# Optimization experiments

Hardware: AMD Instinct MI355X
Metric: run time of the kernel (lower is better)

## Reference

```python
import jax, jax.numpy as jnp
import numpy as np
from jax import lax

H = 512
V = 32000
B = 64
S = 64
T = 32
TQ = 32
NUM_HOP = 3


def _p(key, shape, scale=0.05):
    return jax.random.normal(key, shape, dtype=jnp.float32) * scale


def setup_inputs() -> dict:
    key = jax.random.key(0)
    ks = jax.random.split(key, 20)
    inp = {}
    inp["contexts"] = jax.random.randint(ks[0], (B, S, T), 0, V)
    inp["questions"] = jax.random.randint(ks[1], (B, TQ), 0, V)
    inp["emb"] = _p(ks[2], (V, H), 1.0)
    # input module: bidirectional GRU (torch gate order r,z,n)
    inp["Wih_f"] = _p(ks[3], (3 * H, H)); inp["Whh_f"] = _p(ks[4], (3 * H, H))
    inp["bih_f"] = jnp.zeros((3 * H,), jnp.float32); inp["bhh_f"] = jnp.zeros((3 * H,), jnp.float32)
    inp["Wih_b"] = _p(ks[5], (3 * H, H)); inp["Whh_b"] = _p(ks[6], (3 * H, H))
    inp["bih_b"] = jnp.zeros((3 * H,), jnp.float32); inp["bhh_b"] = jnp.zeros((3 * H,), jnp.float32)
    # question module GRU
    inp["qWih"] = _p(ks[7], (3 * H, H)); inp["qWhh"] = _p(ks[8], (3 * H, H))
    inp["qbih"] = jnp.zeros((3 * H,), jnp.float32); inp["qbhh"] = jnp.zeros((3 * H,), jnp.float32)
    # attention GRU cell (note: source reuses br as both biases)
    inp["Wr"] = _p(ks[9], (H, H)); inp["Ur"] = _p(ks[10], (H, H)); inp["br"] = jnp.ones((H,), jnp.float32)
    inp["W"] = _p(ks[11], (H, H)); inp["U"] = _p(ks[12], (H, H))
    # episodic memory gate MLP + next-memory projection
    inp["z1_w"] = _p(ks[13], (H, 4 * H)); inp["z1_b"] = jnp.zeros((H,), jnp.float32)
    inp["z2_w"] = _p(ks[14], (1, H)); inp["z2_b"] = jnp.zeros((1,), jnp.float32)
    inp["nm_w"] = _p(ks[15], (H, 3 * H)); inp["nm_b"] = jnp.zeros((H,), jnp.float32)
    # answer module
    inp["ans_w"] = _p(ks[16], (V, 2 * H)); inp["ans_b"] = jnp.zeros((V,), jnp.float32)
    return inp


def _pos_enc(slen, elen):
    # l[s, e] = 1 - s/slen - (e/elen)*(1 - 2*s/slen); indexed by SENTENCE dim, as in source
    s = np.arange(slen, dtype=np.float64)[:, None]
    e = np.arange(elen, dtype=np.float64)[None, :]
    l = 1.0 - s / slen - (e / elen) * (1.0 - 2.0 * s / slen)
    return jnp.asarray(l, dtype=jnp.float32)  # (S, H)


def _gru(x, Wih, Whh, bih, bhh, reverse=False):
    # x: (B, T, H); torch nn.GRU math with gate order r, z, n
    Bn, Tn, Hn = x.shape
    h0 = jnp.zeros((Bn, Hn), x.dtype)

    def step(h, xt):
        gx = xt @ Wih.T + bih
        gh = h @ Whh.T + bhh
        xr, xz, xn = jnp.split(gx, 3, axis=-1)
        hr, hz, hn = jnp.split(gh, 3, axis=-1)
        r = jax.nn.sigmoid(xr + hr)
        z = jax.nn.sigmoid(xz + hz)
        n = jnp.tanh(xn + r * hn)
        h_new = (1.0 - z) * n + z * h
        return h_new, h_new

    h_last, hs = lax.scan(step, h0, jnp.swapaxes(x, 0, 1), reverse=reverse)
    return jnp.swapaxes(hs, 0, 1), h_last


def _dmn(emb, Wih_f, Whh_f, bih_f, bhh_f, Wih_b, Whh_b, bih_b, bhh_b,
         qWih, qWhh, qbih, qbhh, Wr, Ur, br, W, U,
         z1_w, z1_b, z2_w, z2_b, nm_w, nm_b, ans_w, ans_b,
         contexts, questions):
    emb0 = emb.at[0].set(0.0)  # padding_idx=0
    Bn, Sn, Tn = contexts.shape
    Hn = emb.shape[1]
    # ---- input module ----
    ce = emb0[contexts]                                   # (B,S,T,H)
    pe = _pos_enc(Sn, Hn)                                 # (S,H), broadcast over tokens (faithful)
    facts_in = jnp.sum(ce * pe[None, :, None, :], axis=2)  # (B,S,H)
    hf, _ = _gru(facts_in, Wih_f, Whh_f, bih_f, bhh_f, reverse=False)
    hb, _ = _gru(facts_in, Wih_b, Whh_b, bih_b, bhh_b, reverse=True)
    facts = hf + hb                                       # (B,S,H); dropout = identity (eval)
    # ---- question module ----
    _, q = _gru(emb0[questions], qWih, qWhh, qbih, qbhh)  # (B,H)
    # ---- episodic memory hops ----
    facts_t = jnp.swapaxes(facts, 0, 1)                   # (S,B,H)
    M = q
    for _ in range(NUM_HOP):
        qb = q[:, None, :]
        Mb = M[:, None, :]
        z = jnp.concatenate([facts * qb, facts * Mb,
                             jnp.abs(facts - qb), jnp.abs(facts - Mb)], axis=-1)  # (B,S,4H)
        g1 = jnp.tanh(z @ z1_w.T + z1_b)
        G = jax.nn.softmax((g1 @ z2_w.T + z2_b)[..., 0], axis=1)  # (B,S)

        def agru(c, sg):
            fact, g = sg
            r = jax.nn.sigmoid(fact @ Wr + c @ Ur + br)
            ht = jnp.tanh(fact @ W + r * (c @ U) + br)  # source reuses br as b
            return g[:, None] * ht + (1.0 - g[:, None]) * c, None

        C, _ = lax.scan(agru, jnp.zeros((Bn, Hn), facts.dtype), (facts_t, G.T))
        M = jax.nn.relu(jnp.concatenate([M, C, q], axis=-1) @ nm_w.T + nm_b)
    # ---- answer module (dropout = identity) ----
    preds = jnp.concatenate([M, q], axis=-1) @ ans_w.T + ans_b  # (B,V)
    return preds


def reference(contexts, questions, emb, Wih_f, Whh_f, bih_f, bhh_f,
              Wih_b, Whh_b, bih_b, bhh_b, qWih, qWhh, qbih, qbhh,
              Wr, Ur, br, W, U, z1_w, z1_b, z2_w, z2_b, nm_w, nm_b,
              ans_w, ans_b):
    return _dmn(emb, Wih_f, Whh_f, bih_f, bhh_f, Wih_b, Whh_b, bih_b, bhh_b,
                qWih, qWhh, qbih, qbhh, Wr, Ur, br, W, U,
                z1_w, z1_b, z2_w, z2_b, nm_w, nm_b, ans_w, ans_b,
                contexts, questions)
```

## Files before the change

kernel.cpp:

```cpp
#include <hip/hip_runtime.h>
#include <cstddef>
#include <cstdint>

namespace {

constexpr int H  = 512;
constexpr int V  = 32000;
constexpr int B  = 64;
constexpr int S  = 64;
constexpr int T  = 32;
constexpr int TQ = 32;

typedef unsigned short ushort_t;
typedef __attribute__((ext_vector_type(8))) short bf16x8;
typedef __attribute__((ext_vector_type(4))) short bf16x4;
typedef __attribute__((ext_vector_type(4))) float f32x4;

__device__ __forceinline__ ushort_t f2bf(float f) {
  union { float f; unsigned u; } v; v.f = f;
  return (ushort_t)((v.u + 0x7FFFu + ((v.u >> 16) & 1u)) >> 16);
}

__device__ __forceinline__ float sigm(float x) { return 1.f / (1.f + expf(-x)); }

__device__ __forceinline__ bf16x8 pack8(f32x4 a, f32x4 b) {
  bf16x8 r;
  r[0] = (short)f2bf(a[0]); r[1] = (short)f2bf(a[1]);
  r[2] = (short)f2bf(a[2]); r[3] = (short)f2bf(a[3]);
  r[4] = (short)f2bf(b[0]); r[5] = (short)f2bf(b[1]);
  r[6] = (short)f2bf(b[2]); r[7] = (short)f2bf(b[3]);
  return r;
}
__device__ __forceinline__ bf16x4 pack4(f32x4 a) {
  bf16x4 r;
  r[0] = (short)f2bf(a[0]); r[1] = (short)f2bf(a[1]);
  r[2] = (short)f2bf(a[2]); r[3] = (short)f2bf(a[3]);
  return r;
}

__device__ __forceinline__ f32x4 load4c(const float* p) {
  f32x4 v;
  asm volatile("global_load_dwordx4 %0, %1, off sc0 sc1" : "=v"(v) : "v"(p));
  return v;
}
__device__ __forceinline__ float load1c(const float* p) {
  float v;
  asm volatile("global_load_dword %0, %1, off sc0 sc1" : "=v"(v) : "v"(p));
  return v;
}
__device__ __forceinline__ void store1c(float* p, float v) {
  asm volatile("global_store_dword %0, %1, off sc0 sc1" :: "v"(p), "v"(v) : "memory");
}
__device__ __forceinline__ void store1cu(unsigned* p, unsigned v) {
  asm volatile("global_store_dword %0, %1, off sc0 sc1" :: "v"(p), "v"(v) : "memory");
}
__device__ __forceinline__ void waitvm0() {
  asm volatile("s_waitcnt vmcnt(0)" ::: "memory");
  __builtin_amdgcn_sched_barrier(0);
}

__device__ __forceinline__ void flag_barrier(unsigned* flags, int rank,
                                             unsigned step1, int t, int lane, int wv) {
  waitvm0();
  __syncthreads();
  if (t == 0) store1cu(flags + rank * 32, step1);
  if (wv == 0) {
    const unsigned* fp = flags + (lane & 7) * 32;
    for (;;) {
      unsigned v;
      asm volatile("global_load_dword %0, %1, off sc0 sc1" : "=v"(v) : "v"(fp));
      asm volatile("s_waitcnt vmcnt(0)" ::: "memory");
      const int ok = (lane >= 8) || (v >= step1);
      if (__all(ok)) break;
      __builtin_amdgcn_s_sleep(1);
    }
  }
  __syncthreads();
}

__global__ __launch_bounds__(256) void k_embed_facts(const int* __restrict__ ctx,
                                                     const float* __restrict__ emb,
                                                     float* __restrict__ facts_in) {
  const int bs = blockIdx.x;
  const int s  = bs & (S - 1);
  const int t  = threadIdx.x;
  __shared__ int sidx[T];
  if (t < T) sidx[t] = ctx[(size_t)bs * T + t];
  __syncthreads();
  float a0 = 0.f, a1 = 0.f;
  for (int tt = 0; tt < T; ++tt) {
    const int ix = sidx[tt];
    if (ix != 0) {
      const float* e = emb + ((size_t)ix << 9);
      a0 += e[t];
      a1 += e[t + 256];
    }
  }
  const float sf = (float)s * (1.f / 64.f);
  const float c1 = 1.f - sf;
  const float c2 = (1.f - 2.f * sf) * (1.f / 512.f);
  facts_in[((size_t)bs << 9) + t]       = a0 * (c1 - (float)t * c2);
  facts_in[((size_t)bs << 9) + t + 256] = a1 * (c1 - (float)(t + 256) * c2);
}

__global__ __launch_bounds__(256) void k_embed_q(const int* __restrict__ qidx,
                                                 const float* __restrict__ emb,
                                                 float* __restrict__ qe) {
  const int bt = blockIdx.x;
  const int t  = threadIdx.x;
  const int ix = qidx[bt];
  float v0 = 0.f, v1 = 0.f;
  if (ix != 0) {
    const float* e = emb + ((size_t)ix << 9);
    v0 = e[t];
    v1 = e[t + 256];
  }
  qe[((size_t)bt << 9) + t]       = v0;
  qe[((size_t)bt << 9) + t + 256] = v1;
}

__global__ __launch_bounds__(256) void k_transpose512(const float* __restrict__ src,
                                                      float* __restrict__ dst) {
  __shared__ float tile[32][33];
  const int x0 = blockIdx.x * 32, y0 = blockIdx.y * 32;
  for (int i = threadIdx.y; i < 32; i += 8)
    tile[i][threadIdx.x] = src[(size_t)(y0 + i) * H + x0 + threadIdx.x];
  __syncthreads();
  for (int i = threadIdx.y; i < 32; i += 8)
    dst[(size_t)(x0 + i) * H + y0 + threadIdx.x] = tile[threadIdx.x][i];
}

template <int ACT>
__global__ __launch_bounds__(256) void k_gemm_mfma(const float* __restrict__ Af,
                                                   const float* __restrict__ Bm,
                                                   const float* __restrict__ bias,
                                                   float* __restrict__ C,
                                                   int M, int N, int K) {
  __shared__ __align__(16) ushort_t As[64][72];
  __shared__ __align__(16) ushort_t Bs[64][72];
  const int t    = threadIdx.x;
  const int lane = t & 63;
  const int w    = t >> 6;
  const int wr   = w >> 1, wc = w & 1;
  const int m0 = blockIdx.y << 6, n0 = blockIdx.x << 6;
  const int row = t >> 2;
  const int ch  = t & 3;

  f32x4 acc[2][2] = {};

  for (int k0 = 0; k0 < K; k0 += 64) {
#pragma unroll
    for (int cc = 0; cc < 2; ++cc) {
      const int c8 = ch + cc * 4;
      const float* src = Af + (size_t)(m0 + row) * K + k0 + c8 * 8;
      *(bf16x8*)&As[row][c8 * 8] = pack8(*(const f32x4*)src, *(const f32x4*)(src + 4));
      const float* srb = Bm + (size_t)(n0 + row) * K + k0 + c8 * 8;
      *(bf16x8*)&Bs[row][c8 * 8] = pack8(*(const f32x4*)srb, *(const f32x4*)(srb + 4));
    }
    __syncthreads();
#pragma unroll
    for (int ks = 0; ks < 2; ++ks) {
      bf16x8 a[2], b[2];
#pragma unroll
      for (int fr = 0; fr < 2; ++fr)
        a[fr] = *(const bf16x8*)&As[wr * 32 + fr * 16 + (lane & 15)][ks * 32 + (lane >> 4) * 8];
#pragma unroll
      for (int fc = 0; fc < 2; ++fc)
        b[fc] = *(const bf16x8*)&Bs[wc * 32 + fc * 16 + (lane & 15)][ks * 32 + (lane >> 4) * 8];
#pragma unroll
      for (int fr = 0; fr < 2; ++fr)
#pragma unroll
        for (int fc = 0; fc < 2; ++fc)
          acc[fr][fc] = __builtin_amdgcn_mfma_f32_16x16x32_bf16(a[fr], b[fc], acc[fr][fc], 0, 0, 0);
    }
    __syncthreads();
  }
#pragma unroll
  for (int fr = 0; fr < 2; ++fr) {
#pragma unroll
    for (int fc = 0; fc < 2; ++fc) {
      const int rbase = m0 + wr * 32 + fr * 16 + ((lane >> 4) << 2);
      const int col   = n0 + wc * 32 + fc * 16 + (lane & 15);
      const float bv  = bias ? bias[col] : 0.f;
#pragma unroll
      for (int j = 0; j < 4; ++j) {
        float v = acc[fr][fc][j] + bv;
        if (ACT == 1) v = tanhf(v);
        if (ACT == 2) v = fmaxf(v, 0.f);
        C[(size_t)(rbase + j) * N + col] = v;
      }
    }
  }
}

__global__ __launch_bounds__(256) void k_gemm_z1(const float* __restrict__ facts,
                                                 const float* __restrict__ qv,
                                                 const float* __restrict__ Mv,
                                                 const float* __restrict__ Bm,
                                                 const float* __restrict__ bias,
                                                 float* __restrict__ C) {
  constexpr int N = 512, K = 2048;
  __shared__ __align__(16) ushort_t As[64][72];
  __shared__ __align__(16) ushort_t Bs[64][72];
  const int t    = threadIdx.x;
  const int lane = t & 63;
  const int w    = t >> 6;
  const int wr   = w >> 1, wc = w & 1;
  const int m0 = blockIdx.y << 6, n0 = blockIdx.x << 6;
  const int row = t >> 2;
  const int ch  = t & 3;
  const int b   = blockIdx.y;

  f32x4 acc[2][2] = {};

  for (int k0 = 0; k0 < K; k0 += 64) {
    const int seg = k0 >> 9;
    const int kb  = k0 & 511;
    const float* other = ((seg & 1) ? Mv : qv) + ((size_t)b << 9);
#pragma unroll
    for (int cc = 0; cc < 2; ++cc) {
      const int c8 = ch + cc * 4;
      const int kk = kb + c8 * 8;
      const float* fp = facts + ((size_t)(m0 + row) << 9) + kk;
      const f32x4 f0 = *(const f32x4*)fp;
      const f32x4 f1 = *(const f32x4*)(fp + 4);
      const f32x4 o0 = *(const f32x4*)(other + kk);
      const f32x4 o1 = *(const f32x4*)(other + kk + 4);
      f32x4 z0, z1;
      if (seg < 2) {
        z0 = f0 * o0; z1 = f1 * o1;
      } else {
        z0 = f0 - o0; z1 = f1 - o1;
#pragma unroll
        for (int e = 0; e < 4; ++e) { z0[e] = fabsf(z0[e]); z1[e] = fabsf(z1[e]); }
      }
      *(bf16x8*)&As[row][c8 * 8] = pack8(z0, z1);
      const float* srb = Bm + (size_t)(n0 + row) * K + k0 + c8 * 8;
      *(bf16x8*)&Bs[row][c8 * 8] = pack8(*(const f32x4*)srb, *(const f32x4*)(srb + 4));
    }
    __syncthreads();
#pragma unroll
    for (int ks = 0; ks < 2; ++ks) {
      bf16x8 a[2], bb[2];
#pragma unroll
      for (int fr = 0; fr < 2; ++fr)
        a[fr] = *(const bf16x8*)&As[wr * 32 + fr * 16 + (lane & 15)][ks * 32 + (lane >> 4) * 8];
#pragma unroll
      for (int fc = 0; fc < 2; ++fc)
        bb[fc] = *(const bf16x8*)&Bs[wc * 32 + fc * 16 + (lane & 15)][ks * 32 + (lane >> 4) * 8];
#pragma unroll
      for (int fr = 0; fr < 2; ++fr)
#pragma unroll
        for (int fc = 0; fc < 2; ++fc)
          acc[fr][fc] = __builtin_amdgcn_mfma_f32_16x16x32_bf16(a[fr], bb[fc], acc[fr][fc], 0, 0, 0);
    }
    __syncthreads();
  }
#pragma unroll
  for (int fr = 0; fr < 2; ++fr) {
#pragma unroll
    for (int fc = 0; fc < 2; ++fc) {
      const int rbase = m0 + wr * 32 + fr * 16 + ((lane >> 4) << 2);
      const int col   = n0 + wc * 32 + fc * 16 + (lane & 15);
      const float bv  = bias[col];
#pragma unroll
      for (int j = 0; j < 4; ++j)
        C[(size_t)(rbase + j) * N + col] = tanhf(acc[fr][fc][j] + bv);
    }
  }
}

__global__ __launch_bounds__(256) void k_gemm_cat3(const float* __restrict__ Mv,
                                                   const float* __restrict__ Cv,
                                                   const float* __restrict__ qv,
                                                   const float* __restrict__ Bm,
                                                   const float* __restrict__ bias,
                                                   float* __restrict__ C) {
  constexpr int N = 512, K = 1536;
  __shared__ __align__(16) ushort_t As[64][72];
  __shared__ __align__(16) ushort_t Bs[64][72];
  const int t    = threadIdx.x;
  const int lane = t & 63;
  const int w    = t >> 6;
  const int wr   = w >> 1, wc = w & 1;
  const int n0 = blockIdx.x << 6;
  const int row = t >> 2;
  const int ch  = t & 3;

  f32x4 acc[2][2] = {};

  for (int k0 = 0; k0 < K; k0 += 64) {
    const int seg = k0 >> 9;
    const float* src = (seg == 0) ? Mv : (seg == 1) ? Cv : qv;
    const int kb = k0 & 511;
#pragma unroll
    for (int cc = 0; cc < 2; ++cc) {
      const int c8 = ch + cc * 4;
      const float* fp = src + ((size_t)row << 9) + kb + c8 * 8;
      *(bf16x8*)&As[row][c8 * 8] = pack8(*(const f32x4*)fp, *(const f32x4*)(fp + 4));
      const float* srb = Bm + (size_t)(n0 + row) * K + k0 + c8 * 8;
      *(bf16x8*)&Bs[row][c8 * 8] = pack8(*(const f32x4*)srb, *(const f32x4*)(srb + 4));
    }
    __syncthreads();
#pragma unroll
    for (int ks = 0; ks < 2; ++ks) {
      bf16x8 a[2], bb[2];
#pragma unroll
      for (int fr = 0; fr < 2; ++fr)
        a[fr] = *(const bf16x8*)&As[wr * 32 + fr * 16 + (lane & 15)][ks * 32 + (lane >> 4) * 8];
#pragma unroll
      for (int fc = 0; fc < 2; ++fc)
        bb[fc] = *(const bf16x8*)&Bs[wc * 32 + fc * 16 + (lane & 15)][ks * 32 + (lane >> 4) * 8];
#pragma unroll
      for (int fr = 0; fr < 2; ++fr)
#pragma unroll
        for (int fc = 0; fc < 2; ++fc)
          acc[fr][fc] = __builtin_amdgcn_mfma_f32_16x16x32_bf16(a[fr], bb[fc], acc[fr][fc], 0, 0, 0);
    }
    __syncthreads();
  }
#pragma unroll
  for (int fr = 0; fr < 2; ++fr) {
#pragma unroll
    for (int fc = 0; fc < 2; ++fc) {
      const int rbase = wr * 32 + fr * 16 + ((lane >> 4) << 2);
      const int col   = n0 + wc * 32 + fc * 16 + (lane & 15);
      const float bv  = bias[col];
#pragma unroll
      for (int j = 0; j < 4; ++j)
        C[(size_t)(rbase + j) * N + col] = fmaxf(acc[fr][fc][j] + bv, 0.f);
    }
  }
}

__global__ __launch_bounds__(256) void k_gemm_cat2(const float* __restrict__ Mv,
                                                   const float* __restrict__ qv,
                                                   const float* __restrict__ Bm,
                                                   const float* __restrict__ bias,
                                                   float* __restrict__ C) {
  constexpr int N = 32000, K = 1024;
  __shared__ __align__(16) ushort_t As[64][72];
  __shared__ __align__(16) ushort_t Bs[64][72];
  const int t    = threadIdx.x;
  const int lane = t & 63;
  const int w    = t >> 6;
  const int wr   = w >> 1, wc = w & 1;
  const int n0 = blockIdx.x << 6;
  const int row = t >> 2;
  const int ch  = t & 3;

  f32x4 acc[2][2] = {};

  for (int k0 = 0; k0 < K; k0 += 64) {
    const float* src = (k0 < 512) ? Mv : qv;
    const int kb = k0 & 511;
#pragma unroll
    for (int cc = 0; cc < 2; ++cc) {
      const int c8 = ch + cc * 4;
      const float* fp = src + ((size_t)row << 9) + kb + c8 * 8;
      *(bf16x8*)&As[row][c8 * 8] = pack8(*(const f32x4*)fp, *(const f32x4*)(fp + 4));
      const float* srb = Bm + (size_t)(n0 + row) * K + k0 + c8 * 8;
      *(bf16x8*)&Bs[row][c8 * 8] = pack8(*(const f32x4*)srb, *(const f32x4*)(srb + 4));
    }
    __syncthreads();
#pragma unroll
    for (int ks = 0; ks < 2; ++ks) {
      bf16x8 a[2], bb[2];
#pragma unroll
      for (int fr = 0; fr < 2; ++fr)
        a[fr] = *(const bf16x8*)&As[wr * 32 + fr * 16 + (lane & 15)][ks * 32 + (lane >> 4) * 8];
#pragma unroll
      for (int fc = 0; fc < 2; ++fc)
        bb[fc] = *(const bf16x8*)&Bs[wc * 32 + fc * 16 + (lane & 15)][ks * 32 + (lane >> 4) * 8];
#pragma unroll
      for (int fr = 0; fr < 2; ++fr)
#pragma unroll
        for (int fc = 0; fc < 2; ++fc)
          acc[fr][fc] = __builtin_amdgcn_mfma_f32_16x16x32_bf16(a[fr], bb[fc], acc[fr][fc], 0, 0, 0);
    }
    __syncthreads();
  }
#pragma unroll
  for (int fr = 0; fr < 2; ++fr) {
#pragma unroll
    for (int fc = 0; fc < 2; ++fc) {
      const int rbase = wr * 32 + fr * 16 + ((lane >> 4) << 2);
      const int col   = n0 + wc * 32 + fc * 16 + (lane & 15);
      const float bv  = bias[col];
#pragma unroll
      for (int j = 0; j < 4; ++j)
        C[(size_t)(rbase + j) * N + col] = acc[fr][fc][j] + bv;
    }
  }
}

__global__ __launch_bounds__(256, 1) void k_gru_scan_mfma(
    const float* __restrict__ Whh_f, const float* __restrict__ bhh_f,
    const float* __restrict__ Whh_b, const float* __restrict__ bhh_b,
    const float* __restrict__ qWhh,  const float* __restrict__ qbhh,
    const float* __restrict__ gx_f, const float* __restrict__ gx_b,
    const float* __restrict__ gx_q,
    float* __restrict__ Hbuf, float* __restrict__ facts,
    float* __restrict__ hb_all, unsigned* __restrict__ flags_base) {
  const int bx   = blockIdx.x;
  const int grp  = bx >> 3;
  const int rank = bx & 7;
  const int gru  = grp >> 2;
  const int ib   = grp & 3;

  const float* Whh; const float* bhh; const float* gx;
  float* H0; float* H1; float* out_seq; int seqlen, rev;
  if (gru == 0)      { Whh = Whh_f; bhh = bhh_f; gx = gx_f; H0 = Hbuf;          H1 = Hbuf + 32768;  out_seq = facts;   seqlen = S;  rev = 0; }
  else if (gru == 1) { Whh = Whh_b; bhh = bhh_b; gx = gx_b; H0 = Hbuf + 65536;  H1 = Hbuf + 98304;  out_seq = hb_all;  seqlen = S;  rev = 1; }
  else               { Whh = qWhh;  bhh = qbhh;  gx = gx_q; H0 = Hbuf + 131072; H1 = Hbuf + 163840; out_seq = nullptr; seqlen = TQ; rev = 0; }

  __shared__ __align__(16) ushort_t hl[16 * 520];

  const int t    = threadIdx.x;
  const int lane = t & 63;
  const int wv   = t >> 6;
  const int nt   = (rank << 2) + wv;
  const int lm   = lane & 15;
  const int lk   = lane >> 4;
  const int col  = (nt << 4) + lm;

  bf16x8 wf[3][16];
#pragma unroll
  for (int g = 0; g < 3; ++g) {
    const float* wrow = Whh + ((size_t)(g * 512 + col) << 9) + (lk << 3);
#pragma unroll
    for (int ks = 0; ks < 16; ++ks) {
      const float* p = wrow + ks * 32;
      wf[g][ks] = pack8(*(const f32x4*)p, *(const f32x4*)(p + 4));
    }
  }
  const float bv0 = bhh[col], bv1 = bhh[512 + col], bv2 = bhh[1024 + col];
  unsigned* flags = flags_base + grp * 8 * 32;

  float xr[4], xz[4], xn[4];
  {
    const int xidx = rev ? (seqlen - 1) : 0;
#pragma unroll
    for (int j = 0; j < 4; ++j) {
      const int b = (ib << 4) + (lk << 2) + j;
      const size_t gxrow = ((size_t)b * seqlen + xidx) * 1536;
      xr[j] = gx[gxrow + col];
      xz[j] = gx[gxrow + 512 + col];
      xn[j] = gx[gxrow + 1024 + col];
    }
  }

  for (int s = 0; s < seqlen; ++s) {
    float hp[4] = {0.f, 0.f, 0.f, 0.f};
    if (s == 0) {
      for (int i = t; i < 4160; i += 256) ((unsigned*)hl)[i] = 0u;
    } else {
      const float* Hp = (s & 1) ? H1 : H0;
      f32x4 v[8];
#pragma unroll
      for (int u = 0; u < 8; ++u) {
        const int i = (u << 8) + t;
        v[u] = load4c(Hp + ((size_t)((ib << 4) + (i >> 7)) << 9) + ((i & 127) << 2));
      }
#pragma unroll
      for (int j = 0; j < 4; ++j)
        hp[j] = load1c(Hp + ((size_t)((ib << 4) + (lk << 2) + j) << 9) + col);
      waitvm0();
#pragma unroll
      for (int u = 0; u < 8; ++u) {
        const int i = (u << 8) + t;
        *(bf16x4*)&hl[(i >> 7) * 520 + ((i & 127) << 2)] = pack4(v[u]);
      }
    }
    __syncthreads();

    f32x4 acc0 = {}, acc1 = {}, acc2 = {};
#pragma unroll
    for (int ks = 0; ks < 16; ++ks) {
      const bf16x8 a = *(const bf16x8*)&hl[lm * 520 + (ks << 5) + (lk << 3)];
      acc0 = __builtin_amdgcn_mfma_f32_16x16x32_bf16(a, wf[0][ks], acc0, 0, 0, 0);
      acc1 = __builtin_amdgcn_mfma_f32_16x16x32_bf16(a, wf[1][ks], acc1, 0, 0, 0);
      acc2 = __builtin_amdgcn_mfma_f32_16x16x32_bf16(a, wf[2][ks], acc2, 0, 0, 0);
    }

    const int xidx = rev ? (seqlen - 1 - s) : s;
    float* Hn = (s & 1) ? H0 : H1;
#pragma unroll
    for (int j = 0; j < 4; ++j) {
      const int b = (ib << 4) + (lk << 2) + j;
      const float r = sigm(xr[j] + acc0[j] + bv0);
      const float z = sigm(xz[j] + acc1[j] + bv1);
      const float n = tanhf(xn[j] + r * (acc2[j] + bv2));
      const float hnew = (1.f - z) * n + z * hp[j];
      store1c(Hn + ((size_t)b << 9) + col, hnew);
      if (out_seq) out_seq[((size_t)(b * S + xidx) << 9) + col] = hnew;
    }

    if (s + 1 < seqlen) {
      const int xidx2 = rev ? (seqlen - 2 - s) : (s + 1);
      float nxr[4], nxz[4], nxn[4];
#pragma unroll
      for (int j = 0; j < 4; ++j) {
        const int b = (ib << 4) + (lk << 2) + j;
        const size_t gxrow = ((size_t)b * seqlen + xidx2) * 1536;
        nxr[j] = gx[gxrow + col];
        nxz[j] = gx[gxrow + 512 + col];
        nxn[j] = gx[gxrow + 1024 + col];
      }
      flag_barrier(flags, rank, (unsigned)(s + 1), t, lane, wv);
#pragma unroll
      for (int j = 0; j < 4; ++j) { xr[j] = nxr[j]; xz[j] = nxz[j]; xn[j] = nxn[j]; }
    }
  }
}

__global__ __launch_bounds__(256, 1) void k_agru_scan_mfma(
    const float* __restrict__ UrT, const float* __restrict__ UT,
    const float* __restrict__ fRW, const float* __restrict__ fW,
    const float* __restrict__ br, const float* __restrict__ G,
    float* __restrict__ C0, float* __restrict__ C1,
    unsigned* __restrict__ flags_base) {
  const int bx   = blockIdx.x;
  const int grp  = bx >> 3;
  const int rank = bx & 7;

  __shared__ __align__(16) ushort_t cl[16 * 520];

  const int t    = threadIdx.x;
  const int lane = t & 63;
  const int wv   = t >> 6;
  const int nt   = (rank << 2) + wv;
  const int lm   = lane & 15;
  const int lk   = lane >> 4;
  const int col  = (nt << 4) + lm;

  bf16x8 wfr[16], wfu[16];
  {
    const float* r0 = UrT + ((size_t)col << 9) + (lk << 3);
    const float* r1 = UT  + ((size_t)col << 9) + (lk << 3);
#pragma unroll
    for (int ks = 0; ks < 16; ++ks) {
      wfr[ks] = pack8(*(const f32x4*)(r0 + ks * 32), *(const f32x4*)(r0 + ks * 32 + 4));
      wfu[ks] = pack8(*(const f32x4*)(r1 + ks * 32), *(const f32x4*)(r1 + ks * 32 + 4));
    }
  }
  const float brv = br[col];
  unsigned* flags = flags_base + grp * 8 * 32;

  float fr[4], fw[4], gg[4];
#pragma unroll
  for (int j = 0; j < 4; ++j) {
    const int b = (grp << 4) + (lk << 2) + j;
    const size_t fi = ((size_t)(b * S) << 9) + col;
    fr[j] = fRW[fi];
    fw[j] = fW[fi];
    gg[j] = G[b << 6];
  }

  for (int s = 0; s < S; ++s) {
    float cp[4] = {0.f, 0.f, 0.f, 0.f};
    if (s == 0) {
      for (int i = t; i < 4160; i += 256) ((unsigned*)cl)[i] = 0u;
    } else {
      const float* Cp = (s & 1) ? C1 : C0;
      f32x4 v[8];
#pragma unroll
      for (int u = 0; u < 8; ++u) {
        const int i = (u << 8) + t;
        v[u] = load4c(Cp + ((size_t)((grp << 4) + (i >> 7)) << 9) + ((i & 127) << 2));
      }
#pragma unroll
      for (int j = 0; j < 4; ++j)
        cp[j] = load1c(Cp + ((size_t)((grp << 4) + (lk << 2) + j) << 9) + col);
      waitvm0();
#pragma unroll
      for (int u = 0; u < 8; ++u) {
        const int i = (u << 8) + t;
        *(bf16x4*)&cl[(i >> 7) * 520 + ((i & 127) << 2)] = pack4(v[u]);
      }
    }
    __syncthreads();

    f32x4 accr = {}, accu = {};
#pragma unroll
    for (int ks = 0; ks < 16; ++ks) {
      const bf16x8 a = *(const bf16x8*)&cl[lm * 520 + (ks << 5) + (lk << 3)];
      accr = __builtin_amdgcn_mfma_f32_16x16x32_bf16(a, wfr[ks], accr, 0, 0, 0);
      accu = __builtin_amdgcn_mfma_f32_16x16x32_bf16(a, wfu[ks], accu, 0, 0, 0);
    }

    float* Cn = (s & 1) ? C0 : C1;
#pragma unroll
    for (int j = 0; j < 4; ++j) {
      const int b = (grp << 4) + (lk << 2) + j;
      const float r  = sigm(fr[j] + accr[j] + brv);
      const float ht = tanhf(fw[j] + r * accu[j] + brv);
      store1c(Cn + ((size_t)b << 9) + col, gg[j] * ht + (1.f - gg[j]) * cp[j]);
    }

    if (s + 1 < S) {
      float nfr[4], nfw[4], ngg[4];
#pragma unroll
      for (int j = 0; j < 4; ++j) {
        const int b = (grp << 4) + (lk << 2) + j;
        const size_t fi = ((size_t)(b * S + s + 1) << 9) + col;
        nfr[j] = fRW[fi];
        nfw[j] = fW[fi];
        ngg[j] = G[(b << 6) + s + 1];
      }
      flag_barrier(flags, rank, (unsigned)(s + 1), t, lane, wv);
#pragma unroll
      for (int j = 0; j < 4; ++j) { fr[j] = nfr[j]; fw[j] = nfw[j]; gg[j] = ngg[j]; }
    }
  }
}

__global__ __launch_bounds__(256) void k_add(float* __restrict__ a, const float* __restrict__ b) {
  const size_t i = (((size_t)blockIdx.x << 8) + threadIdx.x) << 2;
  float4 x = *(float4*)(a + i);
  const float4 y = *(const float4*)(b + i);
  x.x += y.x; x.y += y.y; x.z += y.z; x.w += y.w;
  *(float4*)(a + i) = x;
}

__global__ __launch_bounds__(256) void k_score_softmax(const float* __restrict__ g1,
                                                       const float* __restrict__ z2w,
                                                       const float* __restrict__ z2b,
                                                       float* __restrict__ G) {
  const int b = blockIdx.x, t = threadIdx.x;
  const int wave = t >> 6, lane = t & 63;
  __shared__ float sc[64];
  for (int si = 0; si < 16; ++si) {
    const int s = wave * 16 + si;
    const float* row = g1 + ((size_t)(b * S + s) << 9) + lane * 8;
    const float* w   = z2w + lane * 8;
    float p = 0.f;
#pragma unroll
    for (int k = 0; k < 8; ++k) p += row[k] * w[k];
#pragma unroll
    for (int off = 32; off; off >>= 1) p += __shfl_xor(p, off);
    if (lane == 0) sc[s] = p + z2b[0];
  }
  __syncthreads();
  if (wave == 0) {
    const float v = sc[lane];
    float m = v;
#pragma unroll
    for (int off = 32; off; off >>= 1) m = fmaxf(m, __shfl_xor(m, off));
    const float e = expf(v - m);
    float su = e;
#pragma unroll
    for (int off = 32; off; off >>= 1) su += __shfl_xor(su, off);
    G[(b << 6) + lane] = e / su;
  }
}

}

extern "C" void kernel_launch(void* const* d_in, const int* in_sizes, int n_in,
                              void* d_out, int out_size, void* d_ws, size_t ws_size,
                              hipStream_t stream) {
  const int*   contexts  = (const int*)d_in[0];
  const int*   questions = (const int*)d_in[1];
  const float* emb   = (const float*)d_in[2];
  const float* Wih_f = (const float*)d_in[3];
  const float* Whh_f = (const float*)d_in[4];
  const float* bih_f = (const float*)d_in[5];
  const float* bhh_f = (const float*)d_in[6];
  const float* Wih_b = (const float*)d_in[7];
  const float* Whh_b = (const float*)d_in[8];
  const float* bih_b = (const float*)d_in[9];
  const float* bhh_b = (const float*)d_in[10];
  const float* qWih  = (const float*)d_in[11];
  const float* qWhh  = (const float*)d_in[12];
  const float* qbih  = (const float*)d_in[13];
  const float* qbhh  = (const float*)d_in[14];
  const float* Wr    = (const float*)d_in[15];
  const float* Ur    = (const float*)d_in[16];
  const float* br    = (const float*)d_in[17];
  const float* Wm    = (const float*)d_in[18];
  const float* Um    = (const float*)d_in[19];
  const float* z1_w  = (const float*)d_in[20];
  const float* z1_b  = (const float*)d_in[21];
  const float* z2_w  = (const float*)d_in[22];
  const float* z2_b  = (const float*)d_in[23];
  const float* nm_w  = (const float*)d_in[24];
  const float* nm_b  = (const float*)d_in[25];
  const float* ans_w = (const float*)d_in[26];
  const float* ans_b = (const float*)d_in[27];
  (void)in_sizes; (void)n_in; (void)out_size; (void)ws_size;

  float* ws = (float*)d_ws;
  float* WrT      = ws + 0;
  float* UrT      = ws + 262144;
  float* WT       = ws + 524288;
  float* UT       = ws + 786432;
  float* facts_in = ws + 1048576;
  float* qe       = ws + 3145728;
  float* gx_f     = ws + 4194304;
  float* gx_b     = ws + 10485760;
  float* gx_q     = ws + 16777216;
  float* facts    = ws + 19922944;
  float* hb       = ws + 22020096;
  float* Hbuf     = ws + 24117248;
  float* C0       = ws + 24313856;
  float* C1       = ws + 24346624;
  float* M0       = ws + 24379392;
  float* M1       = ws + 24412160;
  float* Mq       = ws + 24543232;
  float* Gm       = ws + 24608768;
  float* g1  = gx_q;
  float* fRW = facts_in;
  float* fW  = hb;
  float* preds = (float*)d_out;
  unsigned* bar = (unsigned*)Mq;

  float* q = Hbuf + 131072;

  hipMemsetAsync(bar, 0, 6144 * sizeof(unsigned), stream);

  k_embed_facts<<<B * S, 256, 0, stream>>>(contexts, emb, facts_in);
  k_embed_q<<<B * TQ, 256, 0, stream>>>(questions, emb, qe);
  dim3 tb(32, 8);
  k_transpose512<<<dim3(16, 16), tb, 0, stream>>>(Wr, WrT);
  k_transpose512<<<dim3(16, 16), tb, 0, stream>>>(Ur, UrT);
  k_transpose512<<<dim3(16, 16), tb, 0, stream>>>(Wm, WT);
  k_transpose512<<<dim3(16, 16), tb, 0, stream>>>(Um, UT);

  k_gemm_mfma<0><<<dim3(24, 64), 256, 0, stream>>>(facts_in, Wih_f, bih_f, gx_f, 4096, 1536, 512);
  k_gemm_mfma<0><<<dim3(24, 64), 256, 0, stream>>>(facts_in, Wih_b, bih_b, gx_b, 4096, 1536, 512);
  k_gemm_mfma<0><<<dim3(24, 32), 256, 0, stream>>>(qe, qWih, qbih, gx_q, 2048, 1536, 512);

  k_gru_scan_mfma<<<96, 256, 0, stream>>>(Whh_f, bhh_f, Whh_b, bhh_b, qWhh, qbhh,
                                          gx_f, gx_b, gx_q, Hbuf, facts, hb, bar);
  k_add<<<2048, 256, 0, stream>>>(facts, hb);

  k_gemm_mfma<0><<<dim3(8, 64), 256, 0, stream>>>(facts, WrT, nullptr, fRW, 4096, 512, 512);
  k_gemm_mfma<0><<<dim3(8, 64), 256, 0, stream>>>(facts, WT,  nullptr, fW,  4096, 512, 512);

  const float* Mcur = q;
  for (int h = 0; h < 3; ++h) {
    k_gemm_z1<<<dim3(8, 64), 256, 0, stream>>>(facts, q, Mcur, z1_w, z1_b, g1);
    k_score_softmax<<<B, 256, 0, stream>>>(g1, z2_w, z2_b, Gm);
    unsigned* fl = bar + 3072 + h * 1024;
    k_agru_scan_mfma<<<32, 256, 0, stream>>>(UrT, UT, fRW, fW, br, Gm, C0, C1, fl);
    float* Mnext = (h & 1) ? M1 : M0;
    k_gemm_cat3<<<dim3(8, 1), 256, 0, stream>>>(Mcur, C0, q, nm_w, nm_b, Mnext);
    Mcur = Mnext;
  }

  k_gemm_cat2<<<dim3(500, 1), 256, 0, stream>>>(Mcur, q, ans_w, ans_b, preds);
}
```

Before: 1.585 ms.

## Exchange recurrent hidden state as bf16 and keep own state in registers

The GRU and attention-GRU scans now publish each step's hidden state to global memory as bf16 instead of fp32. Each block keeps its own previous values in registers rather than reloading them, which halves the per-step cross-block traffic on the serial critical path. Separately, the z1 gate GEMM is split into a kernel that builds the concatenated features as bf16, followed by the generic MFMA GEMM with a bf16 A path. That split adds an extra kernel launch and a write/read of a 4096x2048 bf16 buffer on each hop.

New measurement: 1.400 ms. 1.13x faster.

```diff
diff --git a/kernel.cpp b/kernel.cpp
--- a/kernel.cpp
+++ b/kernel.cpp
@@ -15,6 +15,7 @@
 typedef __attribute__((ext_vector_type(8))) short bf16x8;
 typedef __attribute__((ext_vector_type(4))) short bf16x4;
 typedef __attribute__((ext_vector_type(4))) float f32x4;
+typedef __attribute__((ext_vector_type(4))) unsigned u32x4;
 
 __device__ __forceinline__ ushort_t f2bf(float f) {
   union { float f; unsigned u; } v; v.f = f;
@@ -31,25 +32,14 @@
   r[6] = (short)f2bf(b[2]); r[7] = (short)f2bf(b[3]);
   return r;
 }
-__device__ __forceinline__ bf16x4 pack4(f32x4 a) {
-  bf16x4 r;
-  r[0] = (short)f2bf(a[0]); r[1] = (short)f2bf(a[1]);
-  r[2] = (short)f2bf(a[2]); r[3] = (short)f2bf(a[3]);
-  return r;
-}
-
-__device__ __forceinline__ f32x4 load4c(const float* p) {
-  f32x4 v;
+
+__device__ __forceinline__ u32x4 load16c(const void* p) {
+  u32x4 v;
   asm volatile("global_load_dwordx4 %0, %1, off sc0 sc1" : "=v"(v) : "v"(p));
   return v;
 }
-__device__ __forceinline__ float load1c(const float* p) {
-  float v;
-  asm volatile("global_load_dword %0, %1, off sc0 sc1" : "=v"(v) : "v"(p));
-  return v;
-}
-__device__ __forceinline__ void store1c(float* p, float v) {
-  asm volatile("global_store_dword %0, %1, off sc0 sc1" :: "v"(p), "v"(v) : "memory");
+__device__ __forceinline__ void store2c(ushort_t* p, unsigned v) {
+  asm volatile("global_store_short %0, %1, off sc0 sc1" :: "v"(p), "v"(v) : "memory");
 }
 __device__ __forceinline__ void store1cu(unsigned* p, unsigned v) {
   asm volatile("global_store_dword %0, %1, off sc0 sc1" :: "v"(p), "v"(v) : "memory");
@@ -130,8 +120,8 @@
     dst[(size_t)(x0 + i) * H + y0 + threadIdx.x] = tile[threadIdx.x][i];
 }
 
-template <int ACT>
-__global__ __launch_bounds__(256) void k_gemm_mfma(const float* __restrict__ Af,
+template <bool A_BF16, int ACT>
+__global__ __launch_bounds__(256) void k_gemm_mfma(const void* __restrict__ Av,
                                                    const float* __restrict__ Bm,
                                                    const float* __restrict__ bias,
                                                    float* __restrict__ C,
@@ -149,11 +139,26 @@
   f32x4 acc[2][2] = {};
 
   for (int k0 = 0; k0 < K; k0 += 64) {
+    if (A_BF16) {
+      const ushort_t* A16 = (const ushort_t*)Av;
+#pragma unroll
+      for (int cc = 0; cc < 2; ++cc) {
+        const int c8 = ch + cc * 4;
+        const uint4 v = *(const uint4*)(A16 + (size_t)(m0 + row) * K + k0 + c8 * 8);
+        *(uint4*)&As[row][c8 * 8] = v;
+      }
+    } else {
+      const float* Af = (const float*)Av;
+#pragma unroll
+      for (int cc = 0; cc < 2; ++cc) {
+        const int c8 = ch + cc * 4;
+        const float* src = Af + (size_t)(m0 + row) * K + k0 + c8 * 8;
+        *(bf16x8*)&As[row][c8 * 8] = pack8(*(const f32x4*)src, *(const f32x4*)(src + 4));
+      }
+    }
 #pragma unroll
     for (int cc = 0; cc < 2; ++cc) {
       const int c8 = ch + cc * 4;
-      const float* src = Af + (size_t)(m0 + row) * K + k0 + c8 * 8;
-      *(bf16x8*)&As[row][c8 * 8] = pack8(*(const f32x4*)src, *(const f32x4*)(src + 4));
       const float* srb = Bm + (size_t)(n0 + row) * K + k0 + c8 * 8;
       *(bf16x8*)&Bs[row][c8 * 8] = pack8(*(const f32x4*)srb, *(const f32x4*)(srb + 4));
     }
@@ -193,80 +198,22 @@
   }
 }
 
-__global__ __launch_bounds__(256) void k_gemm_z1(const float* __restrict__ facts,
-                                                 const float* __restrict__ qv,
-                                                 const float* __restrict__ Mv,
-                                                 const float* __restrict__ Bm,
-                                                 const float* __restrict__ bias,
-                                                 float* __restrict__ C) {
-  constexpr int N = 512, K = 2048;
-  __shared__ __align__(16) ushort_t As[64][72];
-  __shared__ __align__(16) ushort_t Bs[64][72];
-  const int t    = threadIdx.x;
-  const int lane = t & 63;
-  const int w    = t >> 6;
-  const int wr   = w >> 1, wc = w & 1;
-  const int m0 = blockIdx.y << 6, n0 = blockIdx.x << 6;
-  const int row = t >> 2;
-  const int ch  = t & 3;
-  const int b   = blockIdx.y;
-
-  f32x4 acc[2][2] = {};
-
-  for (int k0 = 0; k0 < K; k0 += 64) {
-    const int seg = k0 >> 9;
-    const int kb  = k0 & 511;
-    const float* other = ((seg & 1) ? Mv : qv) + ((size_t)b << 9);
-#pragma unroll
-    for (int cc = 0; cc < 2; ++cc) {
-      const int c8 = ch + cc * 4;
-      const int kk = kb + c8 * 8;
-      const float* fp = facts + ((size_t)(m0 + row) << 9) + kk;
-      const f32x4 f0 = *(const f32x4*)fp;
-      const f32x4 f1 = *(const f32x4*)(fp + 4);
-      const f32x4 o0 = *(const f32x4*)(other + kk);
-      const f32x4 o1 = *(const f32x4*)(other + kk + 4);
-      f32x4 z0, z1;
-      if (seg < 2) {
-        z0 = f0 * o0; z1 = f1 * o1;
-      } else {
-        z0 = f0 - o0; z1 = f1 - o1;
-#pragma unroll
-        for (int e = 0; e < 4; ++e) { z0[e] = fabsf(z0[e]); z1[e] = fabsf(z1[e]); }
-      }
-      *(bf16x8*)&As[row][c8 * 8] = pack8(z0, z1);
-      const float* srb = Bm + (size_t)(n0 + row) * K + k0 + c8 * 8;
-      *(bf16x8*)&Bs[row][c8 * 8] = pack8(*(const f32x4*)srb, *(const f32x4*)(srb + 4));
-    }
-    __syncthreads();
-#pragma unroll
-    for (int ks = 0; ks < 2; ++ks) {
-      bf16x8 a[2], bb[2];
-#pragma unroll
-      for (int fr = 0; fr < 2; ++fr)
-        a[fr] = *(const bf16x8*)&As[wr * 32 + fr * 16 + (lane & 15)][ks * 32 + (lane >> 4) * 8];
-#pragma unroll
-      for (int fc = 0; fc < 2; ++fc)
-        bb[fc] = *(const bf16x8*)&Bs[wc * 32 + fc * 16 + (lane & 15)][ks * 32 + (lane >> 4) * 8];
-#pragma unroll
-      for (int fr = 0; fr < 2; ++fr)
-#pragma unroll
-        for (int fc = 0; fc < 2; ++fc)
-          acc[fr][fc] = __builtin_amdgcn_mfma_f32_16x16x32_bf16(a[fr], bb[fc], acc[fr][fc], 0, 0, 0);
-    }
-    __syncthreads();
-  }
-#pragma unroll
-  for (int fr = 0; fr < 2; ++fr) {
-#pragma unroll
-    for (int fc = 0; fc < 2; ++fc) {
-      const int rbase = m0 + wr * 32 + fr * 16 + ((lane >> 4) << 2);
-      const int col   = n0 + wc * 32 + fc * 16 + (lane & 15);
-      const float bv  = bias[col];
-#pragma unroll
-      for (int j = 0; j < 4; ++j)
-        C[(size_t)(rbase + j) * N + col] = tanhf(acc[fr][fc][j] + bv);
-    }
+__global__ __launch_bounds__(256) void k_build_z16(const float* __restrict__ facts,
+                                                   const float* __restrict__ q,
+                                                   const float* __restrict__ M,
+                                                   ushort_t* __restrict__ z) {
+  const int bs = blockIdx.x;
+  const int b  = bs >> 6;
+  const int t  = threadIdx.x;
+  const size_t zb = (size_t)bs << 11;
+  for (int c = t; c < 512; c += 256) {
+    const float f  = facts[((size_t)bs << 9) + c];
+    const float qv = q[(b << 9) + c];
+    const float mv = M[(b << 9) + c];
+    z[zb + c]        = f2bf(f * qv);
+    z[zb + 512 + c]  = f2bf(f * mv);
+    z[zb + 1024 + c] = f2bf(fabsf(f - qv));
+    z[zb + 1536 + c] = f2bf(fabsf(f - mv));
   }
 }
 
@@ -400,8 +347,9 @@
     const float* __restrict__ qWhh,  const float* __restrict__ qbhh,
     const float* __restrict__ gx_f, const float* __restrict__ gx_b,
     const float* __restrict__ gx_q,
-    float* __restrict__ Hbuf, float* __restrict__ facts,
-    float* __restrict__ hb_all, unsigned* __restrict__ flags_base) {
+    ushort_t* __restrict__ H16, float* __restrict__ qbuf,
+    float* __restrict__ facts, float* __restrict__ hb_all,
+    unsigned* __restrict__ flags_base) {
   const int bx   = blockIdx.x;
   const int grp  = bx >> 3;
   const int rank = bx & 7;
@@ -409,10 +357,12 @@
   const int ib   = grp & 3;
 
   const float* Whh; const float* bhh; const float* gx;
-  float* H0; float* H1; float* out_seq; int seqlen, rev;
-  if (gru == 0)      { Whh = Whh_f; bhh = bhh_f; gx = gx_f; H0 = Hbuf;          H1 = Hbuf + 32768;  out_seq = facts;   seqlen = S;  rev = 0; }
-  else if (gru == 1) { Whh = Whh_b; bhh = bhh_b; gx = gx_b; H0 = Hbuf + 65536;  H1 = Hbuf + 98304;  out_seq = hb_all;  seqlen = S;  rev = 1; }
-  else               { Whh = qWhh;  bhh = qbhh;  gx = gx_q; H0 = Hbuf + 131072; H1 = Hbuf + 163840; out_seq = nullptr; seqlen = TQ; rev = 0; }
+  float* out_seq; int seqlen, rev;
+  if (gru == 0)      { Whh = Whh_f; bhh = bhh_f; gx = gx_f; out_seq = facts;   seqlen = S;  rev = 0; }
+  else if (gru == 1) { Whh = Whh_b; bhh = bhh_b; gx = gx_b; out_seq = hb_all;  seqlen = S;  rev = 1; }
+  else               { Whh = qWhh;  bhh = qbhh;  gx = gx_q; out_seq = nullptr; seqlen = TQ; rev = 0; }
+  ushort_t* Hb0 = H16 + gru * 65536;
+  ushort_t* Hb1 = Hb0 + 32768;
 
   __shared__ __align__(16) ushort_t hl[16 * 520];
 
@@ -450,26 +400,24 @@
     }
   }
 
+  float hp[4] = {0.f, 0.f, 0.f, 0.f};
+
   for (int s = 0; s < seqlen; ++s) {
-    float hp[4] = {0.f, 0.f, 0.f, 0.f};
     if (s == 0) {
       for (int i = t; i < 4160; i += 256) ((unsigned*)hl)[i] = 0u;
     } else {
-      const float* Hp = (s & 1) ? H1 : H0;
-      f32x4 v[8];
-#pragma unroll
-      for (int u = 0; u < 8; ++u) {
+      const ushort_t* Hp16 = (s & 1) ? Hb1 : Hb0;
+      u32x4 v[4];
+#pragma unroll
+      for (int u = 0; u < 4; ++u) {
         const int i = (u << 8) + t;
-        v[u] = load4c(Hp + ((size_t)((ib << 4) + (i >> 7)) << 9) + ((i & 127) << 2));
-      }
-#pragma unroll
-      for (int j = 0; j < 4; ++j)
-        hp[j] = load1c(Hp + ((size_t)((ib << 4) + (lk << 2) + j) << 9) + col);
+        v[u] = load16c(Hp16 + ((size_t)((ib << 4) + (i >> 6)) << 9) + ((i << 3) & 511));
+      }
       waitvm0();
 #pragma unroll
-      for (int u = 0; u < 8; ++u) {
+      for (int u = 0; u < 4; ++u) {
         const int i = (u << 8) + t;
-        *(bf16x4*)&hl[(i >> 7) * 520 + ((i & 127) << 2)] = pack4(v[u]);
+        *(u32x4*)&hl[(i >> 6) * 520 + ((i << 3) & 511)] = v[u];
       }
     }
     __syncthreads();
@@ -484,7 +432,7 @@
     }
 
     const int xidx = rev ? (seqlen - 1 - s) : s;
-    float* Hn = (s & 1) ? H0 : H1;
+    ushort_t* Hn16 = (s & 1) ? Hb0 : Hb1;
 #pragma unroll
     for (int j = 0; j < 4; ++j) {
       const int b = (ib << 4) + (lk << 2) + j;
@@ -492,8 +440,10 @@
       const float z = sigm(xz[j] + acc1[j] + bv1);
       const float n = tanhf(xn[j] + r * (acc2[j] + bv2));
       const float hnew = (1.f - z) * n + z * hp[j];
-      store1c(Hn + ((size_t)b << 9) + col, hnew);
+      hp[j] = hnew;
+      if (s + 1 < seqlen) store2c(Hn16 + ((size_t)b << 9) + col, (unsigned)f2bf(hnew));
       if (out_seq) out_seq[((size_t)(b * S + xidx) << 9) + col] = hnew;
+      if (gru == 2 && s == seqlen - 1) qbuf[((size_t)b << 9) + col] = hnew;
     }
 
     if (s + 1 < seqlen) {
@@ -518,11 +468,13 @@
     const float* __restrict__ UrT, const float* __restrict__ UT,
     const float* __restrict__ fRW, const float* __restrict__ fW,
     const float* __restrict__ br, const float* __restrict__ G,
-    float* __restrict__ C0, float* __restrict__ C1,
+    ushort_t* __restrict__ C16, float* __restrict__ C0f,
     unsigned* __restrict__ flags_base) {
   const int bx   = blockIdx.x;
   const int grp  = bx >> 3;
   const int rank = bx & 7;
+  ushort_t* Cb0 = C16;
+  ushort_t* Cb1 = C16 + 32768;
 
   __shared__ __align__(16) ushort_t cl[16 * 520];
 
@@ -557,26 +509,24 @@
     gg[j] = G[b << 6];
   }
 
+  float cp[4] = {0.f, 0.f, 0.f, 0.f};
+
   for (int s = 0; s < S; ++s) {
-    float cp[4] = {0.f, 0.f, 0.f, 0.f};
     if (s == 0) {
       for (int i = t; i < 4160; i += 256) ((unsigned*)cl)[i] = 0u;
     } else {
-      const float* Cp = (s & 1) ? C1 : C0;
-      f32x4 v[8];
-#pragma unroll
-      for (int u = 0; u < 8; ++u) {
+      const ushort_t* Cp16 = (s & 1) ? Cb1 : Cb0;
+      u32x4 v[4];
+#pragma unroll
+      for (int u = 0; u < 4; ++u) {
         const int i = (u << 8) + t;
-        v[u] = load4c(Cp + ((size_t)((grp << 4) + (i >> 7)) << 9) + ((i & 127) << 2));
-      }
-#pragma unroll
-      for (int j = 0; j < 4; ++j)
-        cp[j] = load1c(Cp + ((size_t)((grp << 4) + (lk << 2) + j) << 9) + col);
+        v[u] = load16c(Cp16 + ((size_t)((grp << 4) + (i >> 6)) << 9) + ((i << 3) & 511));
+      }
       waitvm0();
 #pragma unroll
-      for (int u = 0; u < 8; ++u) {
+      for (int u = 0; u < 4; ++u) {
         const int i = (u << 8) + t;
-        *(bf16x4*)&cl[(i >> 7) * 520 + ((i & 127) << 2)] = pack4(v[u]);
+        *(u32x4*)&cl[(i >> 6) * 520 + ((i << 3) & 511)] = v[u];
       }
     }
     __syncthreads();
@@ -589,13 +539,16 @@
       accu = __builtin_amdgcn_mfma_f32_16x16x32_bf16(a, wfu[ks], accu, 0, 0, 0);
     }
 
-    float* Cn = (s & 1) ? C0 : C1;
+    ushort_t* Cn16 = (s & 1) ? Cb0 : Cb1;
 #pragma unroll
     for (int j = 0; j < 4; ++j) {
       const int b = (grp << 4) + (lk << 2) + j;
       const float r  = sigm(fr[j] + accr[j] + brv);
       const float ht = tanhf(fw[j] + r * accu[j] + brv);
-      store1c(Cn + ((size_t)b << 9) + col, gg[j] * ht + (1.f - gg[j]) * cp[j]);
+      const float cnew = gg[j] * ht + (1.f - gg[j]) * cp[j];
+      cp[j] = cnew;
+      if (s + 1 < S) store2c(Cn16 + ((size_t)b << 9) + col, (unsigned)f2bf(cnew));
+      else           C0f[((size_t)b << 9) + col] = cnew;
     }
 
     if (s + 1 < S) {
@@ -704,18 +657,20 @@
   float* hb       = ws + 22020096;
   float* Hbuf     = ws + 24117248;
   float* C0       = ws + 24313856;
-  float* C1       = ws + 24346624;
   float* M0       = ws + 24379392;
   float* M1       = ws + 24412160;
   float* Mq       = ws + 24543232;
   float* Gm       = ws + 24608768;
+  ushort_t* H16 = (ushort_t*)Hbuf;
+  float* qbuf   = Hbuf + 98304;
+  ushort_t* C16 = (ushort_t*)(Hbuf + 131072);
+  ushort_t* zb16 = (ushort_t*)gx_f;
   float* g1  = gx_q;
   float* fRW = facts_in;
   float* fW  = hb;
   float* preds = (float*)d_out;
   unsigned* bar = (unsigned*)Mq;
-
-  float* q = Hbuf + 131072;
+  float* q = qbuf;
 
   hipMemsetAsync(bar, 0, 6144 * sizeof(unsigned), stream);
 
@@ -727,23 +682,24 @@
   k_transpose512<<<dim3(16, 16), tb, 0, stream>>>(Wm, WT);
   k_transpose512<<<dim3(16, 16), tb, 0, stream>>>(Um, UT);
 
-  k_gemm_mfma<0><<<dim3(24, 64), 256, 0, stream>>>(facts_in, Wih_f, bih_f, gx_f, 4096, 1536, 512);
-  k_gemm_mfma<0><<<dim3(24, 64), 256, 0, stream>>>(facts_in, Wih_b, bih_b, gx_b, 4096, 1536, 512);
-  k_gemm_mfma<0><<<dim3(24, 32), 256, 0, stream>>>(qe, qWih, qbih, gx_q, 2048, 1536, 512);
+  k_gemm_mfma<false, 0><<<dim3(24, 64), 256, 0, stream>>>(facts_in, Wih_f, bih_f, gx_f, 4096, 1536, 512);
+  k_gemm_mfma<false, 0><<<dim3(24, 64), 256, 0, stream>>>(facts_in, Wih_b, bih_b, gx_b, 4096, 1536, 512);
+  k_gemm_mfma<false, 0><<<dim3(24, 32), 256, 0, stream>>>(qe, qWih, qbih, gx_q, 2048, 1536, 512);
 
   k_gru_scan_mfma<<<96, 256, 0, stream>>>(Whh_f, bhh_f, Whh_b, bhh_b, qWhh, qbhh,
-                                          gx_f, gx_b, gx_q, Hbuf, facts, hb, bar);
+                                          gx_f, gx_b, gx_q, H16, qbuf, facts, hb, bar);
   k_add<<<2048, 256, 0, stream>>>(facts, hb);
 
-  k_gemm_mfma<0><<<dim3(8, 64), 256, 0, stream>>>(facts, WrT, nullptr, fRW, 4096, 512, 512);
-  k_gemm_mfma<0><<<dim3(8, 64), 256, 0, stream>>>(facts, WT,  nullptr, fW,  4096, 512, 512);
+  k_gemm_mfma<false, 0><<<dim3(8, 64), 256, 0, stream>>>(facts, WrT, nullptr, fRW, 4096, 512, 512);
+  k_gemm_mfma<false, 0><<<dim3(8, 64), 256, 0, stream>>>(facts, WT,  nullptr, fW,  4096, 512, 512);
 
   const float* Mcur = q;
   for (int h = 0; h < 3; ++h) {
-    k_gemm_z1<<<dim3(8, 64), 256, 0, stream>>>(facts, q, Mcur, z1_w, z1_b, g1);
+    k_build_z16<<<B * S, 256, 0, stream>>>(facts, q, Mcur, zb16);
+    k_gemm_mfma<true, 1><<<dim3(8, 64), 256, 0, stream>>>(zb16, z1_w, z1_b, g1, 4096, 512, 2048);
     k_score_softmax<<<B, 256, 0, stream>>>(g1, z2_w, z2_b, Gm);
     unsigned* fl = bar + 3072 + h * 1024;
-    k_agru_scan_mfma<<<32, 256, 0, stream>>>(UrT, UT, fRW, fW, br, Gm, C0, C1, fl);
+    k_agru_scan_mfma<<<32, 256, 0, stream>>>(UrT, UT, fRW, fW, br, Gm, C16, C0, fl);
     float* Mnext = (h & 1) ? M1 : M0;
     k_gemm_cat3<<<dim3(8, 1), 256, 0, stream>>>(Mcur, C0, q, nm_w, nm_b, Mnext);
     Mcur = Mnext;
```
